# Kernel optimization log

Hardware: AMD Instinct MI355X
Metric: run time of the kernel (lower is better)

The kernel has to match this reference:

```python
import jax, jax.numpy as jnp
import numpy as np


def setup_inputs() -> dict:
    key = jax.random.key(0)
    x = jax.random.normal(key, (16384, 4096), dtype=jnp.float32)
    return {"x": x, "k": 64}


def reference(x, k):
    # allow_negative_topk=False -> select and output based on ReLU(x)
    scores = jax.nn.relu(x)                      # [N, D]
    kk = min(k, scores.shape[-1])
    _, topk_idx = jax.lax.top_k(scores, kk)      # [N, kk]
    rows = jnp.arange(scores.shape[0])[:, None]  # [N, 1]
    mask = jnp.zeros_like(scores).at[rows, topk_idx].set(1.0)
    return scores * mask
```

## Files before the change

kernel.cpp:

```cpp
#include <hip/hip_runtime.h>


constexpr int ROW_LEN = 4096;
constexpr int TPB     = 256;
constexpr int EPT     = ROW_LEN / TPB;

__global__ __launch_bounds__(TPB, 4)
void topk_relu_kernel(const float* __restrict__ x, const int* __restrict__ kptr,
                      float* __restrict__ out, int rows)
{
    __shared__ int hist[256];
    __shared__ int wtot[4];
    __shared__ int sel_digit;
    __shared__ int sel_kk;
    __shared__ int sel_flag;

    const int row = blockIdx.x;
    if (row >= rows) return;
    const int tid  = threadIdx.x;
    const int lane = tid & 63;
    const int wid  = tid >> 6;

    const size_t rowbase = (size_t)row * ROW_LEN + (size_t)tid * EPT;
    const float4* __restrict__ xv = (const float4*)(x + rowbase);

    unsigned int key[EPT];
#pragma unroll
    for (int j = 0; j < EPT / 4; ++j) {
        float4 v = xv[j];
        key[4 * j + 0] = __float_as_uint(fmaxf(v.x, 0.0f));
        key[4 * j + 1] = __float_as_uint(fmaxf(v.y, 0.0f));
        key[4 * j + 2] = __float_as_uint(fmaxf(v.z, 0.0f));
        key[4 * j + 3] = __float_as_uint(fmaxf(v.w, 0.0f));
    }

    int k = *kptr;
    if (k > ROW_LEN) k = ROW_LEN;

    const unsigned int KPRE_BITS = 0x3FC00000u;
    int c1 = 0;
#pragma unroll
    for (int j = 0; j < EPT; ++j) c1 += (key[j] > KPRE_BITS) ? 1 : 0;
#pragma unroll
    for (int d = 1; d < 64; d <<= 1) c1 += __shfl_down(c1, d);
    if (lane == 0) wtot[wid] = c1;
    __syncthreads();
    const int cpre = wtot[0] + wtot[1] + wtot[2] + wtot[3];
    const unsigned int kpre = (cpre >= k) ? KPRE_BITS : 0u;

    int kk = k;
    unsigned int prefix = 0;
    int t0flag = 0;

    for (int p = 0; p < 4; ++p) {
        const int shift = 24 - 8 * p;
        hist[tid] = 0;
        if (tid == 0) sel_flag = 0;
        __syncthreads();
#pragma unroll
        for (int j = 0; j < EPT; ++j) {
            const unsigned int kj = key[j];
            if (kj > kpre && (p == 0 || (kj >> (shift + 8)) == prefix))
                atomicAdd(&hist[(kj >> shift) & 255u], 1);
        }
        __syncthreads();
        if (tid < 64) {
            const int b0 = tid * 4;
            const int h0 = hist[b0 + 0], h1 = hist[b0 + 1];
            const int h2 = hist[b0 + 2], h3 = hist[b0 + 3];
            const int lsum = h0 + h1 + h2 + h3;
            int suf = lsum;
#pragma unroll
            for (int d = 1; d < 64; d <<= 1) {
                int v = __shfl_down(suf, d);
                if (lane < 64 - d) suf += v;
            }
            const unsigned long long m = __ballot(suf >= kk);
            if (m == 0ull) {
                if (lane == 0) sel_flag = 1;
            } else {
                const int L = 63 - __clzll(m);
                if (lane == L) {
                    int cum = suf - lsum;
                    const int hh[4] = {h0, h1, h2, h3};
#pragma unroll
                    for (int b = 3; b >= 0; --b) {
                        const int h = hh[b];
                        if (cum + h >= kk) { sel_digit = b0 + b; sel_kk = kk - cum; break; }
                        cum += h;
                    }
                }
            }
        }
        __syncthreads();
        if (sel_flag) { t0flag = 1; break; }
        prefix = (prefix << 8) | (unsigned int)sel_digit;
        kk = sel_kk;
        __syncthreads();
    }

    unsigned int T;
    int need;
    if (t0flag) { T = 0u; need = 0; }
    else        { T = prefix; need = kk; }

    int eqc = 0;
#pragma unroll
    for (int j = 0; j < EPT; ++j) eqc += (key[j] == T) ? 1 : 0;
    int inc = eqc;
#pragma unroll
    for (int d = 1; d < 64; d <<= 1) {
        int v = __shfl_up(inc, d);
        if (lane >= d) inc += v;
    }
    if (lane == 63) wtot[wid] = inc;
    __syncthreads();
    int base = 0;
    for (int w = 0; w < wid; ++w) base += wtot[w];
    int r = base + (inc - eqc);

    float4* __restrict__ ov = (float4*)(out + rowbase);
#pragma unroll
    for (int j = 0; j < EPT / 4; ++j) {
        float4 v;
        float f[4];
#pragma unroll
        for (int c = 0; c < 4; ++c) {
            const unsigned int kj = key[4 * j + c];
            bool keep;
            if (kj == T) { keep = (r < need); ++r; }
            else         { keep = (kj > T); }
            f[c] = keep ? __uint_as_float(kj) : 0.0f;
        }
        v.x = f[0]; v.y = f[1]; v.z = f[2]; v.w = f[3];
        ov[j] = v;
    }
}

extern "C" void kernel_launch(void* const* d_in, const int* in_sizes, int n_in,
                              void* d_out, int out_size, void* d_ws, size_t ws_size,
                              hipStream_t stream)
{
    const float* x    = (const float*)d_in[0];
    const int*   kptr = (const int*)d_in[1];
    float*       out  = (float*)d_out;
    const int rows = in_sizes[0] / ROW_LEN;
    topk_relu_kernel<<<rows, TPB, 0, stream>>>(x, kptr, out, rows);
}
```

Before: 120.6 us.

## Persistent grid with next-row prefetch and LDS candidate compaction for radix select

Switches to a persistent grid of up to 1024 blocks that loop over rows. Each block prefetches the next row into registers while it processes the current one. Values above a fixed threshold are compacted into a small LDS buffer, and a single wave runs the 4-pass radix select on that buffer using wave-level shuffles instead of block barriers. It also adds nontemporal loads and stores and lighter LDS-only barriers. If the candidate count falls outside [k, 512], it falls back to the full block radix select. The costs are extra register pressure from the prefetch buffer and reliance on the threshold usually yielding few candidates.

```diff
diff --git a/kernel.cpp b/kernel.cpp
--- a/kernel.cpp
+++ b/kernel.cpp
@@ -4,136 +4,238 @@
 constexpr int ROW_LEN = 4096;
 constexpr int TPB     = 256;
 constexpr int EPT     = ROW_LEN / TPB;
+constexpr int CAP     = 512;
+constexpr unsigned int KPRE_BITS = 0x3FC00000u;
+
+typedef float f32x4 __attribute__((ext_vector_type(4)));
+
+__device__ __forceinline__ void bar_lds() {
+    asm volatile("s_waitcnt lgkmcnt(0)" ::: "memory");
+    __builtin_amdgcn_sched_barrier(0);
+    __builtin_amdgcn_s_barrier();
+}
 
 __global__ __launch_bounds__(TPB, 4)
 void topk_relu_kernel(const float* __restrict__ x, const int* __restrict__ kptr,
                       float* __restrict__ out, int rows)
 {
-    __shared__ int hist[256];
+    __shared__ unsigned int cand[CAP];
+    __shared__ alignas(16) int hist[256];
+    __shared__ int ccount;
+    __shared__ unsigned int selT;
+    __shared__ int selNeed;
     __shared__ int wtot[4];
-    __shared__ int sel_digit;
-    __shared__ int sel_kk;
-    __shared__ int sel_flag;
-
-    const int row = blockIdx.x;
-    if (row >= rows) return;
+    __shared__ int sel_digit, sel_kk, sel_flag;
+
     const int tid  = threadIdx.x;
     const int lane = tid & 63;
     const int wid  = tid >> 6;
 
-    const size_t rowbase = (size_t)row * ROW_LEN + (size_t)tid * EPT;
-    const float4* __restrict__ xv = (const float4*)(x + rowbase);
-
-    unsigned int key[EPT];
-#pragma unroll
-    for (int j = 0; j < EPT / 4; ++j) {
-        float4 v = xv[j];
-        key[4 * j + 0] = __float_as_uint(fmaxf(v.x, 0.0f));
-        key[4 * j + 1] = __float_as_uint(fmaxf(v.y, 0.0f));
-        key[4 * j + 2] = __float_as_uint(fmaxf(v.z, 0.0f));
-        key[4 * j + 3] = __float_as_uint(fmaxf(v.w, 0.0f));
-    }
-
     int k = *kptr;
     if (k > ROW_LEN) k = ROW_LEN;
 
-    const unsigned int KPRE_BITS = 0x3FC00000u;
-    int c1 = 0;
-#pragma unroll
-    for (int j = 0; j < EPT; ++j) c1 += (key[j] > KPRE_BITS) ? 1 : 0;
-#pragma unroll
-    for (int d = 1; d < 64; d <<= 1) c1 += __shfl_down(c1, d);
-    if (lane == 0) wtot[wid] = c1;
-    __syncthreads();
-    const int cpre = wtot[0] + wtot[1] + wtot[2] + wtot[3];
-    const unsigned int kpre = (cpre >= k) ? KPRE_BITS : 0u;
-
-    int kk = k;
-    unsigned int prefix = 0;
-    int t0flag = 0;
-
-    for (int p = 0; p < 4; ++p) {
-        const int shift = 24 - 8 * p;
-        hist[tid] = 0;
-        if (tid == 0) sel_flag = 0;
-        __syncthreads();
+    int row = blockIdx.x;
+    const int stride = gridDim.x;
+    if (row >= rows) return;
+
+    unsigned int key[EPT];
+    {
+        const f32x4* __restrict__ xv =
+            (const f32x4*)(x + (size_t)row * ROW_LEN + (size_t)tid * EPT);
+#pragma unroll
+        for (int j = 0; j < 4; ++j) {
+            f32x4 v = __builtin_nontemporal_load(&xv[j]);
+#pragma unroll
+            for (int c = 0; c < 4; ++c)
+                key[4 * j + c] = __float_as_uint(fmaxf(v[c], 0.0f));
+        }
+    }
+
+    for (;;) {
+        const int nrow = row + stride;
+        const bool haveNext = (nrow < rows);
+
+        f32x4 pf[4];
+        if (haveNext) {
+            const f32x4* __restrict__ xv =
+                (const f32x4*)(x + (size_t)nrow * ROW_LEN + (size_t)tid * EPT);
+#pragma unroll
+            for (int j = 0; j < 4; ++j) pf[j] = __builtin_nontemporal_load(&xv[j]);
+        }
+
+        if (tid == 0) { ccount = 0; sel_flag = 0; }
+        bar_lds();
+
+        int m = 0;
+#pragma unroll
+        for (int j = 0; j < EPT; ++j) m += (key[j] > KPRE_BITS) ? 1 : 0;
+        int inc = m;
+#pragma unroll
+        for (int d = 1; d < 64; d <<= 1) {
+            int v = __shfl_up(inc, d);
+            if (lane >= d) inc += v;
+        }
+        const int excl = inc - m;
+        const int wt   = __shfl(inc, 63);
+        int wb = 0;
+        if (lane == 0) wb = atomicAdd(&ccount, wt);
+        wb = __shfl(wb, 0);
+        int pos = wb + excl;
 #pragma unroll
         for (int j = 0; j < EPT; ++j) {
-            const unsigned int kj = key[j];
-            if (kj > kpre && (p == 0 || (kj >> (shift + 8)) == prefix))
-                atomicAdd(&hist[(kj >> shift) & 255u], 1);
-        }
-        __syncthreads();
-        if (tid < 64) {
-            const int b0 = tid * 4;
-            const int h0 = hist[b0 + 0], h1 = hist[b0 + 1];
-            const int h2 = hist[b0 + 2], h3 = hist[b0 + 3];
-            const int lsum = h0 + h1 + h2 + h3;
-            int suf = lsum;
-#pragma unroll
-            for (int d = 1; d < 64; d <<= 1) {
-                int v = __shfl_down(suf, d);
-                if (lane < 64 - d) suf += v;
-            }
-            const unsigned long long m = __ballot(suf >= kk);
-            if (m == 0ull) {
-                if (lane == 0) sel_flag = 1;
-            } else {
-                const int L = 63 - __clzll(m);
-                if (lane == L) {
-                    int cum = suf - lsum;
-                    const int hh[4] = {h0, h1, h2, h3};
-#pragma unroll
-                    for (int b = 3; b >= 0; --b) {
-                        const int h = hh[b];
-                        if (cum + h >= kk) { sel_digit = b0 + b; sel_kk = kk - cum; break; }
-                        cum += h;
-                    }
-                }
-            }
-        }
-        __syncthreads();
-        if (sel_flag) { t0flag = 1; break; }
-        prefix = (prefix << 8) | (unsigned int)sel_digit;
-        kk = sel_kk;
-        __syncthreads();
-    }
-
-    unsigned int T;
-    int need;
-    if (t0flag) { T = 0u; need = 0; }
-    else        { T = prefix; need = kk; }
-
-    int eqc = 0;
-#pragma unroll
-    for (int j = 0; j < EPT; ++j) eqc += (key[j] == T) ? 1 : 0;
-    int inc = eqc;
-#pragma unroll
-    for (int d = 1; d < 64; d <<= 1) {
-        int v = __shfl_up(inc, d);
-        if (lane >= d) inc += v;
-    }
-    if (lane == 63) wtot[wid] = inc;
-    __syncthreads();
-    int base = 0;
-    for (int w = 0; w < wid; ++w) base += wtot[w];
-    int r = base + (inc - eqc);
-
-    float4* __restrict__ ov = (float4*)(out + rowbase);
-#pragma unroll
-    for (int j = 0; j < EPT / 4; ++j) {
-        float4 v;
-        float f[4];
-#pragma unroll
-        for (int c = 0; c < 4; ++c) {
-            const unsigned int kj = key[4 * j + c];
-            bool keep;
-            if (kj == T) { keep = (r < need); ++r; }
-            else         { keep = (kj > T); }
-            f[c] = keep ? __uint_as_float(kj) : 0.0f;
-        }
-        v.x = f[0]; v.y = f[1]; v.z = f[2]; v.w = f[3];
-        ov[j] = v;
+            if (key[j] > KPRE_BITS) {
+                if (pos < CAP) cand[pos] = key[j];
+                ++pos;
+            }
+        }
+        bar_lds();
+        const int cnt = ccount;
+
+        unsigned int T;
+        int need;
+
+        if (cnt >= k && cnt <= CAP) {
+            if (wid == 0) {
+                unsigned int c[CAP / 64];
+#pragma unroll
+                for (int i = 0; i < CAP / 64; ++i) {
+                    const int idx = lane + 64 * i;
+                    c[i] = (idx < cnt) ? cand[idx] : 0u;
+                }
+                int kk = k;
+                unsigned int prefix = 0;
+#pragma unroll
+                for (int p = 0; p < 4; ++p) {
+                    const int shift = 24 - 8 * p;
+                    ((int4*)hist)[lane] = make_int4(0, 0, 0, 0);
+#pragma unroll
+                    for (int i = 0; i < CAP / 64; ++i) {
+                        const int idx = lane + 64 * i;
+                        const unsigned int ci = c[i];
+                        if (idx < cnt && (p == 0 || (ci >> (shift + 8)) == prefix))
+                            atomicAdd(&hist[(ci >> shift) & 255u], 1);
+                    }
+                    const int4 h = ((const int4*)hist)[lane];
+                    const int h0 = h.x, h1 = h.y, h2 = h.z, h3 = h.w;
+                    const int lsum = h0 + h1 + h2 + h3;
+                    int suf = lsum;
+#pragma unroll
+                    for (int d = 1; d < 64; d <<= 1) {
+                        int v = __shfl_down(suf, d);
+                        if (lane < 64 - d) suf += v;
+                    }
+                    const unsigned long long mm = __ballot(suf >= kk);
+                    const int L = 63 - __clzll(mm);
+                    int dig = 0, kkn = 0;
+                    if (lane == L) {
+                        int cum = suf - lsum;
+                        const int hh[4] = {h0, h1, h2, h3};
+#pragma unroll
+                        for (int b = 3; b >= 0; --b) {
+                            if (cum + hh[b] >= kk) { dig = lane * 4 + b; kkn = kk - cum; break; }
+                            cum += hh[b];
+                        }
+                    }
+                    dig = __shfl(dig, L);
+                    kk  = __shfl(kkn, L);
+                    prefix = (prefix << 8) | (unsigned int)dig;
+                }
+                if (lane == 0) { selT = prefix; selNeed = kk; }
+            }
+            bar_lds();
+            T = selT;
+            need = selNeed;
+        } else {
+            int kk = k;
+            unsigned int prefix = 0;
+            int t0 = 0;
+            for (int p = 0; p < 4; ++p) {
+                const int shift = 24 - 8 * p;
+                hist[tid] = 0;
+                if (tid == 0) sel_flag = 0;
+                bar_lds();
+#pragma unroll
+                for (int j = 0; j < EPT; ++j) {
+                    const unsigned int kj = key[j];
+                    if (kj != 0u && (p == 0 || (kj >> (shift + 8)) == prefix))
+                        atomicAdd(&hist[(kj >> shift) & 255u], 1);
+                }
+                bar_lds();
+                if (tid < 64) {
+                    const int b0 = tid * 4;
+                    const int h0 = hist[b0 + 0], h1 = hist[b0 + 1];
+                    const int h2 = hist[b0 + 2], h3 = hist[b0 + 3];
+                    const int lsum = h0 + h1 + h2 + h3;
+                    int suf = lsum;
+#pragma unroll
+                    for (int d = 1; d < 64; d <<= 1) {
+                        int v = __shfl_down(suf, d);
+                        if (lane < 64 - d) suf += v;
+                    }
+                    const unsigned long long mm = __ballot(suf >= kk);
+                    if (mm == 0ull) {
+                        if (lane == 0) sel_flag = 1;
+                    } else {
+                        const int L = 63 - __clzll(mm);
+                        if (lane == L) {
+                            int cum = suf - lsum;
+                            const int hh[4] = {h0, h1, h2, h3};
+#pragma unroll
+                            for (int b = 3; b >= 0; --b) {
+                                if (cum + hh[b] >= kk) { sel_digit = b0 + b; sel_kk = kk - cum; break; }
+                                cum += hh[b];
+                            }
+                        }
+                    }
+                }
+                bar_lds();
+                if (sel_flag) { t0 = 1; break; }
+                prefix = (prefix << 8) | (unsigned int)sel_digit;
+                kk = sel_kk;
+                bar_lds();
+            }
+            if (t0) { T = 0u; need = 0; }
+            else    { T = prefix; need = kk; }
+        }
+
+        int eqc = 0;
+#pragma unroll
+        for (int j = 0; j < EPT; ++j) eqc += (key[j] == T) ? 1 : 0;
+        int einc = eqc;
+#pragma unroll
+        for (int d = 1; d < 64; d <<= 1) {
+            int v = __shfl_up(einc, d);
+            if (lane >= d) einc += v;
+        }
+        if (lane == 63) wtot[wid] = einc;
+        bar_lds();
+        int rbase = 0;
+        for (int w = 0; w < wid; ++w) rbase += wtot[w];
+        int rr = rbase + (einc - eqc);
+
+        f32x4* __restrict__ ov = (f32x4*)(out + (size_t)row * ROW_LEN + (size_t)tid * EPT);
+#pragma unroll
+        for (int j = 0; j < 4; ++j) {
+            f32x4 v;
+#pragma unroll
+            for (int c2 = 0; c2 < 4; ++c2) {
+                const unsigned int kj = key[4 * j + c2];
+                const bool eq = (kj == T);
+                const bool keep = (kj > T) || (eq && rr < need);
+                v[c2] = keep ? __uint_as_float(kj) : 0.0f;
+                rr += eq ? 1 : 0;
+            }
+            __builtin_nontemporal_store(v, &ov[j]);
+        }
+
+        if (!haveNext) break;
+        row = nrow;
+#pragma unroll
+        for (int j = 0; j < 4; ++j) {
+#pragma unroll
+            for (int c = 0; c < 4; ++c)
+                key[4 * j + c] = __float_as_uint(fmaxf(pf[j][c], 0.0f));
+        }
     }
 }
 
@@ -145,5 +247,6 @@
     const int*   kptr = (const int*)d_in[1];
     float*       out  = (float*)d_out;
     const int rows = in_sizes[0] / ROW_LEN;
-    topk_relu_kernel<<<rows, TPB, 0, stream>>>(x, kptr, out, rows);
+    int nb = rows < 1024 ? rows : 1024;
+    topk_relu_kernel<<<nb, TPB, 0, stream>>>(x, kptr, out, rows);
 }
```

Result: slower. 214.1 us (+77.5%).
